# Performance work log

Hardware: AMD Instinct MI355X
Metric: run time of the kernel (lower is better)

## Reference

```python
import jax, jax.numpy as jnp
import numpy as np

N = 100000      # nodes
E = 1600000     # edges
D = 64          # latent_dim
H = 4           # num_heads
HID = 256       # hidden_dim of omics generators
OMICS = [20000, 1881, 27000]  # mrna, mirna, methylation output dims


def _layer_norm(x, w, b, eps=1e-5):
    m = jnp.mean(x, axis=-1, keepdims=True)
    v = jnp.var(x, axis=-1, keepdims=True)
    return (x - m) * jax.lax.rsqrt(v + eps) * w + b


def setup_inputs() -> dict:
    key = jax.random.key(0)
    ks = jax.random.split(key, 64)
    ki = iter(range(64))
    def g(shape, scale=0.05):
        return jax.random.normal(ks[next(ki)], shape, dtype=jnp.float32) * scale
    inp = {
        'latent_vectors': jax.random.normal(ks[next(ki)], (N, D), dtype=jnp.float32),
        'edge_index': jax.random.randint(ks[next(ki)], (2, E), 0, N, dtype=jnp.int32),
        # attention graph constructor (weights stored as [in,out], i.e. torch W^T)
        'wq': g((D, D)), 'bq': jnp.zeros((D,), jnp.float32),
        'wk': g((D, D)), 'bk': jnp.zeros((D,), jnp.float32),
        'wv': g((D, D)), 'bv': jnp.zeros((D,), jnp.float32),
        'ln0_w': jnp.ones((D,), jnp.float32), 'ln0_b': jnp.zeros((D,), jnp.float32),
        # two residual GCN layers
        'gcn1_w': g((D, D)), 'gcn1_b': jnp.zeros((D,), jnp.float32),
        'ln1_w': jnp.ones((D,), jnp.float32), 'ln1_b': jnp.zeros((D,), jnp.float32),
        'gcn2_w': g((D, D)), 'gcn2_b': jnp.zeros((D,), jnp.float32),
        'ln2_w': jnp.ones((D,), jnp.float32), 'ln2_b': jnp.zeros((D,), jnp.float32),
    }
    for j, od in enumerate(OMICS):
        inp[f'gw1_{j}'] = g((D, HID))
        inp[f'gb1_{j}'] = jnp.zeros((HID,), jnp.float32)
        inp[f'gw2_{j}'] = g((HID, od))
        inp[f'gb2_{j}'] = jnp.zeros((od,), jnp.float32)
    return inp


def _gcn(x, row, col, dis, w, b):
    h = x @ w                                   # [N, D]
    norm = (dis[row] * dis[col])[:, None]       # [E+N, 1]
    agg = jax.ops.segment_sum(h[row] * norm, col, num_segments=N)
    return agg + b


def reference(latent_vectors, wq, bq, wk, bk, wv, bv, ln0_w, ln0_b,
              gcn1_w, gcn1_b, ln1_w, ln1_b, gcn2_w, gcn2_b, ln2_w, ln2_b,
              gw1_0, gb1_0, gw2_0, gb2_0,
              gw1_1, gb1_1, gw2_1, gb2_1,
              gw1_2, gb1_2, gw2_2, gb2_2,
              edge_index):
    Dh = D // H
    # AttentionGraphConstructor (faithful: seq dim = 1, attention mixes heads)
    q = (latent_vectors @ wq + bq).reshape(N, 1, H, Dh)
    k = (latent_vectors @ wk + bk).reshape(N, 1, H, Dh)
    v = (latent_vectors @ wv + bv).reshape(N, 1, H, Dh)
    scores = jnp.einsum('nsid,nsjd->nsij', q, k) / (Dh ** 0.5)  # [N,1,H,H]
    attn = jax.nn.softmax(scores, axis=-1)
    out = jnp.einsum('nsij,nsjd->nsid', attn, v)                # [N,1,H,Dh]
    x = _layer_norm(out.transpose(0, 2, 1, 3).reshape(N, D), ln0_w, ln0_b)
    # GCN normalization with self-loops: D^-1/2 (A+I) D^-1/2
    loops = jnp.arange(N, dtype=edge_index.dtype)
    row = jnp.concatenate([edge_index[0], loops])
    col = jnp.concatenate([edge_index[1], loops])
    deg = jax.ops.segment_sum(jnp.ones_like(col, dtype=x.dtype), col, num_segments=N)
    dis = jnp.where(deg > 0, jax.lax.rsqrt(jnp.maximum(deg, 1e-12)), 0.0)
    for gw, gb, lw, lb in ((gcn1_w, gcn1_b, ln1_w, ln1_b),
                           (gcn2_w, gcn2_b, ln2_w, ln2_b)):
        h = _gcn(x, row, col, dis, gw, gb)
        x = _layer_norm(x + h, lw, lb)        # residual (in==out dims)
    # per-omics MLP generators on x[i] (dropout = identity in eval)
    gens = ((gw1_0, gb1_0, gw2_0, gb2_0),
            (gw1_1, gb1_1, gw2_1, gb2_1),
            (gw1_2, gb1_2, gw2_2, gb2_2))
    outs = []
    for i, (w1, b1, w2, b2) in enumerate(gens):
        xi = x[i:i + 1]                        # [1, D]
        hi = jax.nn.relu(xi @ w1 + b1)
        outs.append(hi @ w2 + b2)              # [1, od]
    return jnp.concatenate(outs, axis=-1)      # [1, sum(OMICS)]
```

## Files before the change

### kernel.cpp

```cpp
#include <hip/hip_runtime.h>

#define NN 100000
#define NE 1600000
#define HIDN 256
#define OD0 20000
#define OD1 1881
#define OD2 27000
#define OUT_TOTAL (OD0 + OD1 + OD2)
#define NB_OUT ((OUT_TOTAL + 63) / 64)

#define MAXL1 8192
#define MAXS1 112
#define MAXL2 65536
#define MAXS2 8192

#define MASKW 3200
#define XB_LIST 1024

__device__ __forceinline__ float wave_sum64(float v) {
#pragma unroll
    for (int off = 32; off >= 1; off >>= 1) v += __shfl_xor(v, off, 64);
    return v;
}

__device__ __forceinline__ void insert_set(unsigned* mask, int* cnt, int cap,
                                           int* slot, int* list, int n) {
    unsigned bit = 1u << (n & 31);
    unsigned old = atomicOr(&mask[n >> 5], bit);
    if (!(old & bit)) {
        int s = atomicAdd(cnt, 1);
        if (s < cap) { slot[n] = s; list[s] = n; }
    }
}

__global__ void k_init(int4* base, int n4) {
    int i = blockIdx.x * blockDim.x + threadIdx.x;
    int4 z = make_int4(0, 0, 0, 0);
    for (; i < n4; i += gridDim.x * blockDim.x) base[i] = z;
}

__global__ __launch_bounds__(256) void k_scan1(
        const int* __restrict__ erow, const int* __restrict__ ecol,
        int* __restrict__ cnts, unsigned* __restrict__ mask1,
        int* __restrict__ slot1, int* __restrict__ S1, int2* __restrict__ L1) {
    int gid = blockIdx.x * blockDim.x + threadIdx.x;
    if (gid < 3) insert_set(mask1, &cnts[1], MAXS1, slot1, S1, gid);
    for (int i = gid; i < NE / 4; i += gridDim.x * blockDim.x) {
        int4 c4 = ((const int4*)ecol)[i];
        int cs[4] = {c4.x, c4.y, c4.z, c4.w};
#pragma unroll
        for (int u = 0; u < 4; u++) {
            if (cs[u] < 3) {
                int r = erow[i * 4 + u];
                int idx = atomicAdd(&cnts[0], 1);
                if (idx < MAXL1) L1[idx] = make_int2(r, cs[u]);
                insert_set(mask1, &cnts[1], MAXS1, slot1, S1, r);
            }
        }
    }
}

__global__ __launch_bounds__(256) void k_scan2(
        const int* __restrict__ erow, const int* __restrict__ ecol,
        int* __restrict__ cnts, const unsigned* __restrict__ mask1,
        unsigned* __restrict__ mask2, int* __restrict__ slot2,
        int* __restrict__ S2, const int* __restrict__ S1, int2* __restrict__ L2) {
    int gid = blockIdx.x * blockDim.x + threadIdx.x;
    int ns1 = min(cnts[1], MAXS1);
    if (gid < ns1) insert_set(mask2, &cnts[3], MAXS2, slot2, S2, S1[gid]);
    for (int i = gid; i < NE / 4; i += gridDim.x * blockDim.x) {
        int4 c4 = ((const int4*)ecol)[i];
        int cs[4] = {c4.x, c4.y, c4.z, c4.w};
#pragma unroll
        for (int u = 0; u < 4; u++) {
            int c = cs[u];
            if (mask1[c >> 5] & (1u << (c & 31))) {
                int r = erow[i * 4 + u];
                int idx = atomicAdd(&cnts[2], 1);
                if (idx < MAXL2) L2[idx] = make_int2(r, c);
                insert_set(mask2, &cnts[3], MAXS2, slot2, S2, r);
            }
        }
    }
}

#define DX_GRID 256
__global__ __launch_bounds__(256) void k_degx0(
        const int* __restrict__ cnts, const int* __restrict__ ecol,
        const unsigned* __restrict__ mask2, const int* __restrict__ slot2,
        int* __restrict__ degc,
        const int* __restrict__ S2, const float* __restrict__ latent,
        const float* __restrict__ wq, const float* __restrict__ bq,
        const float* __restrict__ wk, const float* __restrict__ bk,
        const float* __restrict__ wv, const float* __restrict__ bv,
        const float* __restrict__ ln0w, const float* __restrict__ ln0b,
        const float* __restrict__ g1w,
        float* __restrict__ x0c, float* __restrict__ h1c) {
    __shared__ float lw[3 * 4096];
    int t = threadIdx.x, b = blockIdx.x;
    int gid = b * 256 + t;
    {
        const float4* s0 = (const float4*)wq;
        const float4* s1 = (const float4*)wk;
        const float4* s2 = (const float4*)wv;
        float4* d0 = (float4*)&lw[0];
        float4* d1 = (float4*)&lw[4096];
        float4* d2 = (float4*)&lw[8192];
        for (int i = t; i < 1024; i += 256) { d0[i] = s0[i]; d1[i] = s1[i]; d2[i] = s2[i]; }
    }
    for (int i = gid; i < NE / 4; i += DX_GRID * 256) {
        int4 c4 = ((const int4*)ecol)[i];
        int cs[4] = {c4.x, c4.y, c4.z, c4.w};
#pragma unroll
        for (int u = 0; u < 4; u++) {
            int c = cs[u];
            if (mask2[c >> 5] & (1u << (c & 31))) {
                int s = slot2[c];
                if ((unsigned)s < MAXS2) atomicAdd(&degc[s], 1);
            }
        }
    }
    __syncthreads();
    int lane = t & 63, wid = t >> 6;
    int nS2 = min(cnts[3], MAXS2);
    for (int s = b * 4 + wid; s < nS2; s += DX_GRID * 4) {
        int n = S2[s];
        float xv = latent[n * 64 + lane];
        float aq = bq[lane], ak = bk[lane], av = bv[lane];
#pragma unroll
        for (int j = 0; j < 64; j++) {
            float xj = __shfl(xv, j, 64);
            aq = fmaf(xj, lw[j * 64 + lane], aq);
            ak = fmaf(xj, lw[4096 + j * 64 + lane], ak);
            av = fmaf(xj, lw[8192 + j * 64 + lane], av);
        }
        int d = lane & 15;
        float sj[4];
#pragma unroll
        for (int j = 0; j < 4; j++) {
            float kv = __shfl(ak, (j << 4) | d, 64);
            float pp = aq * kv;
            pp += __shfl_xor(pp, 1, 64); pp += __shfl_xor(pp, 2, 64);
            pp += __shfl_xor(pp, 4, 64); pp += __shfl_xor(pp, 8, 64);
            sj[j] = pp * 0.25f;
        }
        float mx = fmaxf(fmaxf(sj[0], sj[1]), fmaxf(sj[2], sj[3]));
        float e0 = expf(sj[0] - mx), e1 = expf(sj[1] - mx);
        float e2 = expf(sj[2] - mx), e3 = expf(sj[3] - mx);
        float inv = 1.f / (e0 + e1 + e2 + e3);
        float at[4] = {e0 * inv, e1 * inv, e2 * inv, e3 * inv};
        float o = 0.f;
#pragma unroll
        for (int j = 0; j < 4; j++) {
            float vv = __shfl(av, (j << 4) | d, 64);
            o = fmaf(at[j], vv, o);
        }
        float sum = wave_sum64(o), sq = wave_sum64(o * o);
        float mean = sum * (1.f / 64.f);
        float var = sq * (1.f / 64.f) - mean * mean;
        float x0 = (o - mean) * rsqrtf(var + 1e-5f) * ln0w[lane] + ln0b[lane];
        x0c[s * 64 + lane] = x0;
        float h = 0.f;
#pragma unroll
        for (int j = 0; j < 64; j++) {
            float xj = __shfl(x0, j, 64);
            h = fmaf(xj, g1w[j * 64 + lane], h);
        }
        h1c[s * 64 + lane] = h;
    }
}

__global__ __launch_bounds__(256) void k_x1agg(
        const int* __restrict__ cnts, const int2* __restrict__ L1,
        const int2* __restrict__ L2, const int* __restrict__ S1,
        const int* __restrict__ slot1, const int* __restrict__ slot2,
        const int* __restrict__ degc,
        const float* __restrict__ x0c, const float* __restrict__ h1c,
        const float* __restrict__ g1b, const float* __restrict__ ln1w,
        const float* __restrict__ ln1b, const float* __restrict__ g2w,
        float* __restrict__ agg2, float* __restrict__ x1c3) {
    __shared__ int   s_cnt;
    __shared__ int   s_ea[XB_LIST];
    __shared__ float s_ew[XB_LIST];
    __shared__ float s_part[4][64];
    int t = threadIdx.x, lane = t & 63, wid = t >> 6, b = blockIdx.x;
    int nl1 = min(cnts[0], MAXL1);
    int ns1 = min(cnts[1], MAXS1);
    int nl2 = min(cnts[2], MAXL2);
    if (b >= ns1) return;
    if (t == 0) s_cnt = 0;
    s_part[wid][lane] = 0.f;
    __syncthreads();
    int n = S1[b];
    int sc2 = slot2[n];
    float dc = rsqrtf((float)(degc[sc2] + 1));
    int ntot = nl2 + ns1;
    for (int e = t; e < ntot; e += 256) {
        int r; bool match;
        if (e < nl2) { int2 rc = L2[e]; r = rc.x; match = (slot1[rc.y] == b); }
        else         { r = S1[e - nl2]; match = (e - nl2 == b); }
        if (match) {
            int a = slot2[r];
            if ((unsigned)a < MAXS2) {
                float w = rsqrtf((float)(degc[a] + 1)) * dc;
                int m = atomicAdd(&s_cnt, 1);
                if (m < XB_LIST) { s_ea[m] = a; s_ew[m] = w; }
            }
        }
    }
    __syncthreads();
    int cm = min(s_cnt, XB_LIST);
    for (int m = wid; m < cm; m += 4)
        s_part[wid][lane] += h1c[s_ea[m] * 64 + lane] * s_ew[m];
    __syncthreads();
    if (wid == 0) {
        float agg = s_part[0][lane] + s_part[1][lane] + s_part[2][lane] + s_part[3][lane];
        float v = x0c[sc2 * 64 + lane] + agg + g1b[lane];
        float sum = wave_sum64(v), sq = wave_sum64(v * v);
        float mean = sum * (1.f / 64.f);
        float var = sq * (1.f / 64.f) - mean * mean;
        float x1 = (v - mean) * rsqrtf(var + 1e-5f) * ln1w[lane] + ln1b[lane];
        if (n < 3) x1c3[n * 64 + lane] = x1;
        float h = 0.f;
#pragma unroll
        for (int j = 0; j < 64; j++) {
            float xj = __shfl(x1, j, 64);
            h = fmaf(xj, g2w[j * 64 + lane], h);
        }
        int ntot2 = nl1 + 3;
        for (int e0 = 0; e0 < ntot2; e0 += 64) {
            int e = e0 + lane;
            int match = 0, cc = 0; float wgt = 0.f;
            if (e < ntot2) {
                int r, c;
                if (e < nl1) { int2 rc = L1[e]; r = rc.x; c = rc.y; }
                else { r = c = e - nl1; }
                if (slot1[r] == b) {
                    int sr2 = slot2[r], scc2 = slot2[c];
                    if ((unsigned)sr2 < MAXS2 && (unsigned)scc2 < MAXS2) {
                        wgt = rsqrtf((float)(degc[sr2] + 1)) * rsqrtf((float)(degc[scc2] + 1));
                        match = 1; cc = c;
                    }
                }
            }
            unsigned long long msk = __ballot(match);
            while (msk) {
                int j = __ffsll((unsigned long long)msk) - 1;
                msk &= msk - 1;
                int cj = __shfl(cc, j, 64);
                float wj = __shfl(wgt, j, 64);
                atomicAdd(&agg2[cj * 64 + lane], h * wj);
            }
        }
    }
}

__global__ __launch_bounds__(256) void k_out2(
        const float* __restrict__ x1c3, const float* __restrict__ agg2,
        const float* __restrict__ g2b, const float* __restrict__ ln2w,
        const float* __restrict__ ln2b,
        const float* __restrict__ w10, const float* __restrict__ b10,
        const float* __restrict__ w11, const float* __restrict__ b11,
        const float* __restrict__ w12, const float* __restrict__ b12,
        const float* __restrict__ w20, const float* __restrict__ b20,
        const float* __restrict__ w21, const float* __restrict__ b21,
        const float* __restrict__ w22, const float* __restrict__ b22,
        float* __restrict__ out) {
    __shared__ float s_x2[192];
    __shared__ float s_hg[768];
    __shared__ float part[256];
    int t = threadIdx.x, lane = t & 63, wid = t >> 6;
    if (wid < 3) {
        float v = x1c3[wid * 64 + lane] + agg2[wid * 64 + lane] + g2b[lane];
        float sum = wave_sum64(v), sq = wave_sum64(v * v);
        float mean = sum * (1.f / 64.f);
        float var = sq * (1.f / 64.f) - mean * mean;
        s_x2[wid * 64 + lane] = (v - mean) * rsqrtf(var + 1e-5f) * ln2w[lane] + ln2b[lane];
    }
    __syncthreads();
    {
        const float* W1[3] = {w10, w11, w12};
        const float* B1[3] = {b10, b11, b12};
#pragma unroll
        for (int gi = 0; gi < 3; gi++) {
            float acc = B1[gi][t];
#pragma unroll
            for (int j = 0; j < 64; j++) acc = fmaf(s_x2[gi * 64 + j], W1[gi][j * 256 + t], acc);
            s_hg[gi * 256 + t] = fmaxf(acc, 0.f);
        }
    }
    __syncthreads();
    int o = blockIdx.x * 64 + lane;
    int gi = -1, jj = 0, od = 1;
    const float* w2 = w20;
    if (o < OD0)                 { gi = 0; jj = o;             od = OD0; w2 = w20; }
    else if (o < OD0 + OD1)      { gi = 1; jj = o - OD0;       od = OD1; w2 = w21; }
    else if (o < OUT_TOTAL)      { gi = 2; jj = o - OD0 - OD1; od = OD2; w2 = w22; }
    float acc = 0.f;
    if (gi >= 0) {
        const float* h = &s_hg[gi * 256 + wid * 64];
        const float* wp = &w2[(size_t)(wid * 64) * od + jj];
#pragma unroll 16
        for (int k = 0; k < 64; k++) acc = fmaf(h[k], wp[(size_t)k * od], acc);
    }
    part[t] = acc;
    __syncthreads();
    if (t < 64 && gi >= 0) {
        float r = part[t] + part[t + 64] + part[t + 128] + part[t + 192];
        const float* b2 = (gi == 0) ? b20 : (gi == 1) ? b21 : b22;
        out[o] = r + b2[jj];
    }
}

extern "C" void kernel_launch(void* const* d_in, const int* in_sizes, int n_in,
                              void* d_out, int out_size, void* d_ws, size_t ws_size,
                              hipStream_t stream) {
    (void)in_sizes; (void)n_in; (void)out_size; (void)ws_size;
    const float* latent = (const float*)d_in[0];
    const int*   edges  = (const int*)d_in[1];
    const float* wq  = (const float*)d_in[2];
    const float* bq  = (const float*)d_in[3];
    const float* wk  = (const float*)d_in[4];
    const float* bk  = (const float*)d_in[5];
    const float* wv  = (const float*)d_in[6];
    const float* bv  = (const float*)d_in[7];
    const float* ln0w = (const float*)d_in[8];
    const float* ln0b = (const float*)d_in[9];
    const float* g1w  = (const float*)d_in[10];
    const float* g1b  = (const float*)d_in[11];
    const float* ln1w = (const float*)d_in[12];
    const float* ln1b = (const float*)d_in[13];
    const float* g2w  = (const float*)d_in[14];
    const float* g2b  = (const float*)d_in[15];
    const float* ln2w = (const float*)d_in[16];
    const float* ln2b = (const float*)d_in[17];
    const float* gw1_0 = (const float*)d_in[18];
    const float* gb1_0 = (const float*)d_in[19];
    const float* gw2_0 = (const float*)d_in[20];
    const float* gb2_0 = (const float*)d_in[21];
    const float* gw1_1 = (const float*)d_in[22];
    const float* gb1_1 = (const float*)d_in[23];
    const float* gw2_1 = (const float*)d_in[24];
    const float* gb2_1 = (const float*)d_in[25];
    const float* gw1_2 = (const float*)d_in[26];
    const float* gb1_2 = (const float*)d_in[27];
    const float* gw2_2 = (const float*)d_in[28];
    const float* gb2_2 = (const float*)d_in[29];

    char* ptr = (char*)d_ws;
    auto alloc = [&](size_t bytes) { char* r = ptr; ptr += (bytes + 255) & ~(size_t)255; return r; };
    int*      cnts  = (int*)alloc(64 * 4);
    unsigned* mask1 = (unsigned*)alloc(MASKW * 4);
    unsigned* mask2 = (unsigned*)alloc(MASKW * 4);
    int*      degc  = (int*)alloc((size_t)MAXS2 * 4);
    float*    agg2  = (float*)alloc(192 * 4);
    char*     zero_end = ptr;
    int*      slot1 = (int*)alloc((size_t)NN * 4);
    int*      slot2 = (int*)alloc((size_t)NN * 4);
    int2*     L1    = (int2*)alloc((size_t)MAXL1 * 8);
    int*      S1    = (int*)alloc((size_t)MAXS1 * 4);
    int2*     L2    = (int2*)alloc((size_t)MAXL2 * 8);
    int*      S2    = (int*)alloc((size_t)MAXS2 * 4);
    float*    x0c   = (float*)alloc((size_t)MAXS2 * 64 * 4);
    float*    h1c   = (float*)alloc((size_t)MAXS2 * 64 * 4);
    float*    x1c3  = (float*)alloc(192 * 4);

    const int* erow = edges;
    const int* ecol = edges + NE;
    int zero_n4 = (int)((zero_end - (char*)cnts) / 16);

    const int SCAN_GRID = (NE / 4 + 255) / 256;
    k_init<<<16, 256, 0, stream>>>((int4*)cnts, zero_n4);
    k_scan1<<<SCAN_GRID, 256, 0, stream>>>(erow, ecol, cnts, mask1, slot1, S1, L1);
    k_scan2<<<SCAN_GRID, 256, 0, stream>>>(erow, ecol, cnts, mask1, mask2, slot2, S2, S1, L2);
    k_degx0<<<DX_GRID, 256, 0, stream>>>(cnts, ecol, mask2, slot2, degc, S2, latent,
                                         wq, bq, wk, bk, wv, bv, ln0w, ln0b, g1w, x0c, h1c);
    k_x1agg<<<MAXS1, 256, 0, stream>>>(cnts, L1, L2, S1, slot1, slot2, degc, x0c, h1c,
                                       g1b, ln1w, ln1b, g2w, agg2, x1c3);
    k_out2<<<NB_OUT, 256, 0, stream>>>(x1c3, agg2, g2b, ln2w, ln2b,
                                       gw1_0, gb1_0, gw1_1, gb1_1, gw1_2, gb1_2,
                                       gw2_0, gb2_0, gw2_1, gb2_1, gw2_2, gb2_2,
                                       (float*)d_out);
}
```

Measured before the change: 79.06 us.

## Compute final layernorm and first MLP layer once in last x1agg block

The second layernorm and the three 64x256 first-layer generator matmuls move out of every k_out2 block into the last-finishing block of k_x1agg. That block is found with a threadfence plus an atomic done counter, and it writes the hidden activations to a global buffer. The new k_gemv kernel only loads those 768 values and runs the large second-layer GEMV. This removes the first-layer work that each of the ~763 output blocks used to repeat, at the cost of a serial tail on one block and a done counter that depends on the cnts region being zeroed each launch.

```diff
diff --git a/kernel.cpp b/kernel.cpp
--- a/kernel.cpp
+++ b/kernel.cpp
@@ -178,104 +178,106 @@
         const float* __restrict__ x0c, const float* __restrict__ h1c,
         const float* __restrict__ g1b, const float* __restrict__ ln1w,
         const float* __restrict__ ln1b, const float* __restrict__ g2w,
-        float* __restrict__ agg2, float* __restrict__ x1c3) {
-    __shared__ int   s_cnt;
-    __shared__ int   s_ea[XB_LIST];
-    __shared__ float s_ew[XB_LIST];
-    __shared__ float s_part[4][64];
-    int t = threadIdx.x, lane = t & 63, wid = t >> 6, b = blockIdx.x;
-    int nl1 = min(cnts[0], MAXL1);
-    int ns1 = min(cnts[1], MAXS1);
-    int nl2 = min(cnts[2], MAXL2);
-    if (b >= ns1) return;
-    if (t == 0) s_cnt = 0;
-    s_part[wid][lane] = 0.f;
-    __syncthreads();
-    int n = S1[b];
-    int sc2 = slot2[n];
-    float dc = rsqrtf((float)(degc[sc2] + 1));
-    int ntot = nl2 + ns1;
-    for (int e = t; e < ntot; e += 256) {
-        int r; bool match;
-        if (e < nl2) { int2 rc = L2[e]; r = rc.x; match = (slot1[rc.y] == b); }
-        else         { r = S1[e - nl2]; match = (e - nl2 == b); }
-        if (match) {
-            int a = slot2[r];
-            if ((unsigned)a < MAXS2) {
-                float w = rsqrtf((float)(degc[a] + 1)) * dc;
-                int m = atomicAdd(&s_cnt, 1);
-                if (m < XB_LIST) { s_ea[m] = a; s_ew[m] = w; }
-            }
-        }
-    }
-    __syncthreads();
-    int cm = min(s_cnt, XB_LIST);
-    for (int m = wid; m < cm; m += 4)
-        s_part[wid][lane] += h1c[s_ea[m] * 64 + lane] * s_ew[m];
-    __syncthreads();
-    if (wid == 0) {
-        float agg = s_part[0][lane] + s_part[1][lane] + s_part[2][lane] + s_part[3][lane];
-        float v = x0c[sc2 * 64 + lane] + agg + g1b[lane];
-        float sum = wave_sum64(v), sq = wave_sum64(v * v);
-        float mean = sum * (1.f / 64.f);
-        float var = sq * (1.f / 64.f) - mean * mean;
-        float x1 = (v - mean) * rsqrtf(var + 1e-5f) * ln1w[lane] + ln1b[lane];
-        if (n < 3) x1c3[n * 64 + lane] = x1;
-        float h = 0.f;
-#pragma unroll
-        for (int j = 0; j < 64; j++) {
-            float xj = __shfl(x1, j, 64);
-            h = fmaf(xj, g2w[j * 64 + lane], h);
-        }
-        int ntot2 = nl1 + 3;
-        for (int e0 = 0; e0 < ntot2; e0 += 64) {
-            int e = e0 + lane;
-            int match = 0, cc = 0; float wgt = 0.f;
-            if (e < ntot2) {
-                int r, c;
-                if (e < nl1) { int2 rc = L1[e]; r = rc.x; c = rc.y; }
-                else { r = c = e - nl1; }
-                if (slot1[r] == b) {
-                    int sr2 = slot2[r], scc2 = slot2[c];
-                    if ((unsigned)sr2 < MAXS2 && (unsigned)scc2 < MAXS2) {
-                        wgt = rsqrtf((float)(degc[sr2] + 1)) * rsqrtf((float)(degc[scc2] + 1));
-                        match = 1; cc = c;
-                    }
-                }
-            }
-            unsigned long long msk = __ballot(match);
-            while (msk) {
-                int j = __ffsll((unsigned long long)msk) - 1;
-                msk &= msk - 1;
-                int cj = __shfl(cc, j, 64);
-                float wj = __shfl(wgt, j, 64);
-                atomicAdd(&agg2[cj * 64 + lane], h * wj);
-            }
-        }
-    }
-}
-
-__global__ __launch_bounds__(256) void k_out2(
-        const float* __restrict__ x1c3, const float* __restrict__ agg2,
+        float* __restrict__ agg2, float* __restrict__ x1c3,
         const float* __restrict__ g2b, const float* __restrict__ ln2w,
         const float* __restrict__ ln2b,
         const float* __restrict__ w10, const float* __restrict__ b10,
         const float* __restrict__ w11, const float* __restrict__ b11,
         const float* __restrict__ w12, const float* __restrict__ b12,
-        const float* __restrict__ w20, const float* __restrict__ b20,
-        const float* __restrict__ w21, const float* __restrict__ b21,
-        const float* __restrict__ w22, const float* __restrict__ b22,
-        float* __restrict__ out) {
-    __shared__ float s_x2[192];
-    __shared__ float s_hg[768];
-    __shared__ float part[256];
-    int t = threadIdx.x, lane = t & 63, wid = t >> 6;
+        float* __restrict__ hg, int* __restrict__ done) {
+    __shared__ int   s_cnt;
+    __shared__ int   s_ea[XB_LIST];
+    __shared__ float s_ew[XB_LIST];
+    __shared__ float s_part[4][64];
+    __shared__ int   s_last;
+    __shared__ float s_x2f[192];
+    int t = threadIdx.x, lane = t & 63, wid = t >> 6, b = blockIdx.x;
+    int nl1 = min(cnts[0], MAXL1);
+    int ns1 = min(cnts[1], MAXS1);
+    int nl2 = min(cnts[2], MAXL2);
+    bool active = (b < ns1);
+    if (active) {
+        if (t == 0) s_cnt = 0;
+        s_part[wid][lane] = 0.f;
+        __syncthreads();
+        int n = S1[b];
+        int sc2 = slot2[n];
+        float dc = rsqrtf((float)(degc[sc2] + 1));
+        int ntot = nl2 + ns1;
+        for (int e = t; e < ntot; e += 256) {
+            int r; bool match;
+            if (e < nl2) { int2 rc = L2[e]; r = rc.x; match = (slot1[rc.y] == b); }
+            else         { r = S1[e - nl2]; match = (e - nl2 == b); }
+            if (match) {
+                int a = slot2[r];
+                if ((unsigned)a < MAXS2) {
+                    float w = rsqrtf((float)(degc[a] + 1)) * dc;
+                    int m = atomicAdd(&s_cnt, 1);
+                    if (m < XB_LIST) { s_ea[m] = a; s_ew[m] = w; }
+                }
+            }
+        }
+        __syncthreads();
+        int cm = min(s_cnt, XB_LIST);
+        for (int m = wid; m < cm; m += 4)
+            s_part[wid][lane] += h1c[s_ea[m] * 64 + lane] * s_ew[m];
+        __syncthreads();
+        if (wid == 0) {
+            float agg = s_part[0][lane] + s_part[1][lane] + s_part[2][lane] + s_part[3][lane];
+            float v = x0c[sc2 * 64 + lane] + agg + g1b[lane];
+            float sum = wave_sum64(v), sq = wave_sum64(v * v);
+            float mean = sum * (1.f / 64.f);
+            float var = sq * (1.f / 64.f) - mean * mean;
+            float x1 = (v - mean) * rsqrtf(var + 1e-5f) * ln1w[lane] + ln1b[lane];
+            if (n < 3) x1c3[n * 64 + lane] = x1;
+            float h = 0.f;
+#pragma unroll
+            for (int j = 0; j < 64; j++) {
+                float xj = __shfl(x1, j, 64);
+                h = fmaf(xj, g2w[j * 64 + lane], h);
+            }
+            int ntot2 = nl1 + 3;
+            for (int e0 = 0; e0 < ntot2; e0 += 64) {
+                int e = e0 + lane;
+                int match = 0, cc = 0; float wgt = 0.f;
+                if (e < ntot2) {
+                    int r, c;
+                    if (e < nl1) { int2 rc = L1[e]; r = rc.x; c = rc.y; }
+                    else { r = c = e - nl1; }
+                    if (slot1[r] == b) {
+                        int sr2 = slot2[r], scc2 = slot2[c];
+                        if ((unsigned)sr2 < MAXS2 && (unsigned)scc2 < MAXS2) {
+                            wgt = rsqrtf((float)(degc[sr2] + 1)) * rsqrtf((float)(degc[scc2] + 1));
+                            match = 1; cc = c;
+                        }
+                    }
+                }
+                unsigned long long msk = __ballot(match);
+                while (msk) {
+                    int j = __ffsll((unsigned long long)msk) - 1;
+                    msk &= msk - 1;
+                    int cj = __shfl(cc, j, 64);
+                    float wj = __shfl(wgt, j, 64);
+                    atomicAdd(&agg2[cj * 64 + lane], h * wj);
+                }
+            }
+        }
+        __syncthreads();
+    }
+    __threadfence();
+    if (t == 0) {
+        int v = atomicAdd(done, 1);
+        s_last = (v == (int)gridDim.x - 1) ? 1 : 0;
+    }
+    __syncthreads();
+    if (!s_last) return;
+    __threadfence();
     if (wid < 3) {
         float v = x1c3[wid * 64 + lane] + agg2[wid * 64 + lane] + g2b[lane];
         float sum = wave_sum64(v), sq = wave_sum64(v * v);
         float mean = sum * (1.f / 64.f);
         float var = sq * (1.f / 64.f) - mean * mean;
-        s_x2[wid * 64 + lane] = (v - mean) * rsqrtf(var + 1e-5f) * ln2w[lane] + ln2b[lane];
+        s_x2f[wid * 64 + lane] = (v - mean) * rsqrtf(var + 1e-5f) * ln2w[lane] + ln2b[lane];
     }
     __syncthreads();
     {
@@ -285,12 +287,24 @@
         for (int gi = 0; gi < 3; gi++) {
             float acc = B1[gi][t];
 #pragma unroll
-            for (int j = 0; j < 64; j++) acc = fmaf(s_x2[gi * 64 + j], W1[gi][j * 256 + t], acc);
-            s_hg[gi * 256 + t] = fmaxf(acc, 0.f);
-        }
-    }
+            for (int j = 0; j < 64; j++) acc = fmaf(s_x2f[gi * 64 + j], W1[gi][j * 256 + t], acc);
+            hg[gi * 256 + t] = fmaxf(acc, 0.f);
+        }
+    }
+}
+
+__global__ __launch_bounds__(256) void k_gemv(const float* __restrict__ hg,
+        const float* __restrict__ w20, const float* __restrict__ b20,
+        const float* __restrict__ w21, const float* __restrict__ b21,
+        const float* __restrict__ w22, const float* __restrict__ b22,
+        float* __restrict__ out) {
+    __shared__ float lh[768];
+    __shared__ float part[256];
+    int t = threadIdx.x;
+    lh[t] = hg[t]; lh[t + 256] = hg[t + 256]; lh[t + 512] = hg[t + 512];
     __syncthreads();
-    int o = blockIdx.x * 64 + lane;
+    int tx = t & 63, ty = t >> 6;
+    int o = blockIdx.x * 64 + tx;
     int gi = -1, jj = 0, od = 1;
     const float* w2 = w20;
     if (o < OD0)                 { gi = 0; jj = o;             od = OD0; w2 = w20; }
@@ -298,8 +312,8 @@
     else if (o < OUT_TOTAL)      { gi = 2; jj = o - OD0 - OD1; od = OD2; w2 = w22; }
     float acc = 0.f;
     if (gi >= 0) {
-        const float* h = &s_hg[gi * 256 + wid * 64];
-        const float* wp = &w2[(size_t)(wid * 64) * od + jj];
+        const float* h = &lh[gi * 256 + ty * 64];
+        const float* wp = &w2[(size_t)(ty * 64) * od + jj];
 #pragma unroll 16
         for (int k = 0; k < 64; k++) acc = fmaf(h[k], wp[(size_t)k * od], acc);
     }
@@ -364,6 +378,7 @@
     float*    x0c   = (float*)alloc((size_t)MAXS2 * 64 * 4);
     float*    h1c   = (float*)alloc((size_t)MAXS2 * 64 * 4);
     float*    x1c3  = (float*)alloc(192 * 4);
+    float*    hg    = (float*)alloc(3 * HIDN * 4);
 
     const int* erow = edges;
     const int* ecol = edges + NE;
@@ -376,9 +391,10 @@
     k_degx0<<<DX_GRID, 256, 0, stream>>>(cnts, ecol, mask2, slot2, degc, S2, latent,
                                          wq, bq, wk, bk, wv, bv, ln0w, ln0b, g1w, x0c, h1c);
     k_x1agg<<<MAXS1, 256, 0, stream>>>(cnts, L1, L2, S1, slot1, slot2, degc, x0c, h1c,
-                                       g1b, ln1w, ln1b, g2w, agg2, x1c3);
-    k_out2<<<NB_OUT, 256, 0, stream>>>(x1c3, agg2, g2b, ln2w, ln2b,
+                                       g1b, ln1w, ln1b, g2w, agg2, x1c3,
+                                       g2b, ln2w, ln2b,
                                        gw1_0, gb1_0, gw1_1, gb1_1, gw1_2, gb1_2,
-                                       gw2_0, gb2_0, gw2_1, gb2_1, gw2_2, gb2_2,
+                                       hg, &cnts[8]);
+    k_gemv<<<NB_OUT, 256, 0, stream>>>(hg, gw2_0, gb2_0, gw2_1, gb2_1, gw2_2, gb2_2,
                                        (float*)d_out);
 }
```

Measured after the change: 82.58 us. 4.5% more time.
